# Optimization experiments

Hardware: AMD Instinct MI355X
Metric: run time of the kernel (lower is better)

The kernel has to match this reference:

```python
import jax, jax.numpy as jnp
import numpy as np

ALG = 8  # octonion algebra dimension
_TRIPLES = [(1,2,3),(1,4,5),(1,7,6),(2,4,6),(2,5,7),(3,4,7),(3,6,5)]

def _oct_table():
    # Cayley multiplication table: e_i * e_j = S[i,j] * e_{K[i,j]}
    K = np.zeros((8,8), np.int64); S = np.zeros((8,8), np.int64)
    K[0,:] = np.arange(8); S[0,:] = 1
    K[:,0] = np.arange(8); S[:,0] = 1
    for i in range(1,8):
        K[i,i] = 0; S[i,i] = -1
    for (a,b,c) in _TRIPLES:
        for x,y,z in ((a,b,c),(b,c,a),(c,a,b)):
            K[x,y] = z; S[x,y] = 1
            K[y,x] = z; S[y,x] = -1
    return K, S

_K, _S = _oct_table()

def _ternary(w):
    # BitNet-style absmean ternary quantization (STE is irrelevant for fwd)
    scale = jnp.mean(jnp.abs(w)) + 1e-8
    wq = jnp.clip(jnp.round(w / scale), -1.0, 1.0) * scale
    return w + jax.lax.stop_gradient(wq - w)

def _oct_big(w):
    # w: [8, din8, dout8] -> structured dense [8*din8, 8*dout8]
    # out_k = sum_{i,j: e_i e_j = s e_k} s * x_i @ W_j  (64 static blocks)
    din8, dout8 = w.shape[1], w.shape[2]
    big = jnp.zeros((8, din8, 8, dout8), w.dtype)
    for i in range(8):
        for j in range(8):
            big = big.at[i, :, int(_K[i, j]), :].set(float(_S[i, j]) * w[j])
    return big.reshape(8 * din8, 8 * dout8)

def _oct_linear(x, w):
    return x @ _oct_big(_ternary(w))

def setup_inputs() -> dict:
    key = jax.random.key(0)
    k1, k2, k3, k4 = jax.random.split(key, 4)
    B, T, D = 8, 4096, 768
    H = 2048  # int(2*4*768/3) rounded up to multiple of 8
    d8, h8 = D // ALG, H // ALG
    x = jax.random.normal(k1, (B, T, D), dtype=jnp.float32)
    w_gate = 0.02 * jax.random.normal(k2, (ALG, d8, h8), dtype=jnp.float32)
    w_up   = 0.02 * jax.random.normal(k3, (ALG, d8, h8), dtype=jnp.float32)
    w_down = 0.02 * jax.random.normal(k4, (ALG, h8, d8), dtype=jnp.float32)
    return {"x": x, "w_gate": w_gate, "w_up": w_up, "w_down": w_down}

def reference(x, w_gate, w_up, w_down):
    gate = _oct_linear(x, w_gate)          # [B,T,H]
    up   = _oct_linear(x, w_up)            # [B,T,H]
    h    = jax.nn.silu(gate) * up          # SwiGLU gate
    return _oct_linear(h, w_down)          # [B,T,D]
```

## Files before the change

kernel.cpp:

```cpp
#include <hip/hip_runtime.h>
#include <hip/hip_bf16.h>

typedef unsigned short u16;
typedef unsigned int u32;
typedef float f32x4 __attribute__((ext_vector_type(4)));
typedef __bf16 bf16x8 __attribute__((ext_vector_type(8)));

#define AS1 __attribute__((address_space(1)))
#define AS3 __attribute__((address_space(3)))

#define MTOT 32768
#define DK   768
#define HN   2048

__constant__ signed char J_TAB[64] = {
  0,1,2,3,4,5,6,7,
  1,0,3,2,5,4,7,6,
  2,3,0,1,6,7,4,5,
  3,2,1,0,7,6,5,4,
  4,5,6,7,0,1,2,3,
  5,4,7,6,1,0,3,2,
  6,7,4,5,2,3,0,1,
  7,6,5,4,3,2,1,0};
__constant__ signed char S_TAB[64] = {
   1, 1, 1, 1, 1, 1, 1, 1,
  -1, 1,-1, 1,-1, 1, 1,-1,
  -1, 1, 1,-1,-1,-1, 1, 1,
  -1,-1, 1, 1,-1, 1,-1, 1,
  -1, 1, 1, 1, 1,-1,-1,-1,
  -1,-1, 1,-1, 1, 1, 1,-1,
  -1,-1,-1, 1, 1,-1, 1, 1,
  -1, 1,-1,-1, 1, 1,-1, 1};

__device__ __forceinline__ u16 f2bf(float f) {
  u32 x = __float_as_uint(f);
  x += 0x7fffu + ((x >> 16) & 1u);
  return (u16)(x >> 16);
}

__device__ __forceinline__ void gload_lds16(const void* g, void* l) {
  __builtin_amdgcn_global_load_lds((AS1 void*)(g), (AS3 void*)(l), 16, 0, 0);
}

#define VMW(N) do { __builtin_amdgcn_sched_barrier(0); \
  asm volatile("s_waitcnt vmcnt(" #N ")" ::: "memory"); \
  __builtin_amdgcn_sched_barrier(0); } while (0)
#define BAR() do { __builtin_amdgcn_sched_barrier(0); \
  __builtin_amdgcn_s_barrier(); \
  __builtin_amdgcn_sched_barrier(0); } while (0)

template <int LDK>
__device__ __forceinline__ void stage_half(const u16* __restrict__ src,
                                           u16* lds, int tid) {
#pragma unroll
  for (int f0 = 0; f0 < 1024; f0 += 512) {
    int flat = f0 + tid;
    int row = flat >> 3;
    int c = (flat & 7) ^ (row & 7);
    gload_lds16(src + row * LDK + c * 8, lds + (f0 + (tid & ~63)) * 8);
  }
}

template <int LDK, bool SA, bool SB, int VM>
__device__ __forceinline__ void ktile4(
    const u16* lAp, const u16* lBp, u16* lAn, u16* lBn,
    const u16* __restrict__ aStage, const u16* __restrict__ bStage,
    int tid, int arow, int brow, int c0, int c1, f32x4 (&acc)[8][4]) {
  bf16x8 afr[4][2], bfr[4][2];
#pragma unroll
  for (int mi = 0; mi < 4; ++mi) {
    const u16* p = lAp + (arow + mi * 16) * 64;
    afr[mi][0] = *(const bf16x8*)(p + c0);
    afr[mi][1] = *(const bf16x8*)(p + c1);
  }
#pragma unroll
  for (int ni = 0; ni < 2; ++ni) {
    const u16* p = lBp + (brow + ni * 16) * 64;
    bfr[ni][0] = *(const bf16x8*)(p + c0);
    bfr[ni][1] = *(const bf16x8*)(p + c1);
  }
  if constexpr (SA) stage_half<LDK>(aStage, lAn, tid);
  BAR();
  __builtin_amdgcn_s_setprio(1);
#pragma unroll
  for (int mi = 0; mi < 4; ++mi)
#pragma unroll
    for (int ni = 0; ni < 2; ++ni) {
      acc[mi][ni] = __builtin_amdgcn_mfma_f32_16x16x32_bf16(
          afr[mi][0], bfr[ni][0], acc[mi][ni], 0, 0, 0);
      acc[mi][ni] = __builtin_amdgcn_mfma_f32_16x16x32_bf16(
          afr[mi][1], bfr[ni][1], acc[mi][ni], 0, 0, 0);
    }
  __builtin_amdgcn_s_setprio(0);
  BAR();
#pragma unroll
  for (int ni = 2; ni < 4; ++ni) {
    const u16* p = lBp + (brow + ni * 16) * 64;
    bfr[ni][0] = *(const bf16x8*)(p + c0);
    bfr[ni][1] = *(const bf16x8*)(p + c1);
  }
  if constexpr (SA) stage_half<LDK>(aStage + 128 * LDK, lAn + 128 * 64, tid);
  BAR();
  __builtin_amdgcn_s_setprio(1);
#pragma unroll
  for (int mi = 0; mi < 4; ++mi)
#pragma unroll
    for (int ni = 2; ni < 4; ++ni) {
      acc[mi][ni] = __builtin_amdgcn_mfma_f32_16x16x32_bf16(
          afr[mi][0], bfr[ni][0], acc[mi][ni], 0, 0, 0);
      acc[mi][ni] = __builtin_amdgcn_mfma_f32_16x16x32_bf16(
          afr[mi][1], bfr[ni][1], acc[mi][ni], 0, 0, 0);
    }
  __builtin_amdgcn_s_setprio(0);
  BAR();
#pragma unroll
  for (int mi = 0; mi < 4; ++mi) {
    const u16* p = lAp + (arow + 64 + mi * 16) * 64;
    afr[mi][0] = *(const bf16x8*)(p + c0);
    afr[mi][1] = *(const bf16x8*)(p + c1);
  }
  if constexpr (SB) stage_half<LDK>(bStage, lBn, tid);
  BAR();
  __builtin_amdgcn_s_setprio(1);
#pragma unroll
  for (int mi = 0; mi < 4; ++mi)
#pragma unroll
    for (int ni = 2; ni < 4; ++ni) {
      acc[4 + mi][ni] = __builtin_amdgcn_mfma_f32_16x16x32_bf16(
          afr[mi][0], bfr[ni][0], acc[4 + mi][ni], 0, 0, 0);
      acc[4 + mi][ni] = __builtin_amdgcn_mfma_f32_16x16x32_bf16(
          afr[mi][1], bfr[ni][1], acc[4 + mi][ni], 0, 0, 0);
    }
  __builtin_amdgcn_s_setprio(0);
  BAR();
  if constexpr (SB) stage_half<LDK>(bStage + 128 * LDK, lBn + 128 * 64, tid);
  if constexpr (VM == 4) VMW(4);
  else if constexpr (VM == 0) VMW(0);
  BAR();
  __builtin_amdgcn_s_setprio(1);
#pragma unroll
  for (int mi = 0; mi < 4; ++mi)
#pragma unroll
    for (int ni = 0; ni < 2; ++ni) {
      acc[4 + mi][ni] = __builtin_amdgcn_mfma_f32_16x16x32_bf16(
          afr[mi][0], bfr[ni][0], acc[4 + mi][ni], 0, 0, 0);
      acc[4 + mi][ni] = __builtin_amdgcn_mfma_f32_16x16x32_bf16(
          afr[mi][1], bfr[ni][1], acc[4 + mi][ni], 0, 0, 0);
    }
  __builtin_amdgcn_s_setprio(0);
  BAR();
}

template <int NK, int LDK>
__device__ __forceinline__ void gemm_core(const u16* __restrict__ aSrc,
                                          const u16* __restrict__ bSrc, int tid,
                                          u16* lA0, u16* lA1, u16* lB0, u16* lB1,
                                          f32x4 (&acc)[8][4]) {
  const int lane = tid & 63;
  const int wave = tid >> 6;
  const int wm = wave >> 2, wn = wave & 3;
  const int l15 = lane & 15, quad = (lane >> 4) & 3;
  const int arow = wm * 128 + l15;
  const int brow = wn * 64 + l15;
  const int c0 = (quad ^ (l15 & 7)) * 8;
  const int c1 = ((quad + 4) ^ (l15 & 7)) * 8;

  stage_half<LDK>(aSrc, lA0, tid);
  stage_half<LDK>(aSrc + 128 * LDK, lA0 + 128 * 64, tid);
  stage_half<LDK>(bSrc, lB0, tid);
  stage_half<LDK>(bSrc + 128 * LDK, lB0 + 128 * 64, tid);
  stage_half<LDK>(bSrc + 64, lB1, tid);
  stage_half<LDK>(bSrc + 64 + 128 * LDK, lB1 + 128 * 64, tid);
  VMW(4);
  BAR();

#pragma unroll 1
  for (int i = 0; i < NK / 2 - 1; ++i) {
    ktile4<LDK, true, true, 4>(lA0, lB0, lA1, lB0,
                               aSrc + (2 * i + 1) * 64, bSrc + (2 * i + 2) * 64,
                               tid, arow, brow, c0, c1, acc);
    ktile4<LDK, true, true, 4>(lA1, lB1, lA0, lB1,
                               aSrc + (2 * i + 2) * 64, bSrc + (2 * i + 3) * 64,
                               tid, arow, brow, c0, c1, acc);
  }
  ktile4<LDK, true, false, 0>(lA0, lB0, lA1, lB0,
                              aSrc + (NK - 1) * 64, nullptr,
                              tid, arow, brow, c0, c1, acc);
  ktile4<LDK, false, false, -1>(lA1, lB1, lA0, lB1, nullptr, nullptr,
                                tid, arow, brow, c0, c1, acc);
}

__global__ void scales1_kernel(const float* __restrict__ w0,
                               const float* __restrict__ w1,
                               const float* __restrict__ w2,
                               float* __restrict__ partials) {
  __shared__ float red[256];
  const int t = blockIdx.x / 192;
  const int chunk = blockIdx.x % 192;
  const float* w = (t == 0) ? w0 : (t == 1) ? w1 : w2;
  const float4* w4 = (const float4*)(w + chunk * 1024);
  float4 v = w4[threadIdx.x];
  red[threadIdx.x] = fabsf(v.x) + fabsf(v.y) + fabsf(v.z) + fabsf(v.w);
  __syncthreads();
  for (int off = 128; off; off >>= 1) {
    if (threadIdx.x < off) red[threadIdx.x] += red[threadIdx.x + off];
    __syncthreads();
  }
  if (threadIdx.x == 0) partials[blockIdx.x] = red[0];
}

__global__ void scales2_kernel(const float* __restrict__ partials,
                               float* __restrict__ scales) {
  __shared__ float red[256];
  float s = (threadIdx.x < 192) ? partials[blockIdx.x * 192 + threadIdx.x] : 0.f;
  red[threadIdx.x] = s;
  __syncthreads();
  for (int off = 128; off; off >>= 1) {
    if (threadIdx.x < off) red[threadIdx.x] += red[threadIdx.x + off];
    __syncthreads();
  }
  if (threadIdx.x == 0) scales[blockIdx.x] = red[0] / 196608.f + 1e-8f;
}

__global__ void build_big_kernel(const float* __restrict__ w,
                                 const float* __restrict__ scales, int sidx,
                                 int A, int B, int ilv, u16* __restrict__ dst) {
  int idx = blockIdx.x * 256 + threadIdx.x;
  int K8 = 8 * A;
  int n = idx / K8;
  int k = idx - n * K8;
  int i = k / A, a = k - i * A;
  int c = n / B, b = n - c * B;
  float scale = scales[sidx];
  int j = J_TAB[i * 8 + c];
  float q = rintf(w[(j * A + a) * B + b] / scale);
  q = fminf(1.f, fmaxf(-1.f, q));
  int nd = (ilv < 0) ? n : (((n & ~15) << 1) | (ilv << 4) | (n & 15));
  dst[nd * K8 + k] = f2bf(q * (float)S_TAB[i * 8 + c]);
}

__global__ void cvt_x_kernel(const float* __restrict__ x, u16* __restrict__ xb) {
  int gid = blockIdx.x * 256 + threadIdx.x;
  const float4* x4 = (const float4*)x;
  float4 v0 = x4[gid * 2], v1 = x4[gid * 2 + 1];
  uint4 o;
  o.x = (u32)f2bf(v0.x) | ((u32)f2bf(v0.y) << 16);
  o.y = (u32)f2bf(v0.z) | ((u32)f2bf(v0.w) << 16);
  o.z = (u32)f2bf(v1.x) | ((u32)f2bf(v1.y) << 16);
  o.w = (u32)f2bf(v1.z) | ((u32)f2bf(v1.w) << 16);
  ((uint4*)xb)[gid] = o;
}

__global__ __launch_bounds__(512, 2) void gemm1_kernel(
    const u16* __restrict__ xb, const u16* __restrict__ wgu,
    const float* __restrict__ scales, u16* __restrict__ h) {
  __shared__ __align__(16) u16 lA0[256 * 64], lA1[256 * 64];
  __shared__ __align__(16) u16 lB0[256 * 64], lB1[256 * 64];
  const int tid = threadIdx.x;
  const int logical = (blockIdx.x & 7) * 256 + (blockIdx.x >> 3);
  const int bn = logical & 15;
  const int bm = logical >> 4;
  const int m0 = bm * 256, n0 = bn * 256;

  f32x4 acc[8][4] = {};
  gemm_core<12, DK>(xb + (size_t)m0 * DK, wgu + (size_t)n0 * DK, tid,
                    lA0, lA1, lB0, lB1, acc);

  const int lane = tid & 63, wave = tid >> 6;
  const int wm = wave >> 2, wn = wave & 3;
  const int l15 = lane & 15, quad = lane >> 4;
  const float sg = scales[0], su = scales[1];
  const int hb = bn * 8 + wn * 2;
#pragma unroll
  for (int mi = 0; mi < 8; ++mi)
#pragma unroll
    for (int pr = 0; pr < 2; ++pr) {
      const int hc = (hb + pr) * 16 + l15;
#pragma unroll
      for (int r = 0; r < 4; ++r) {
        int m = m0 + wm * 128 + mi * 16 + quad * 4 + r;
        float g = acc[mi][2 * pr][r] * sg;
        float u = acc[mi][2 * pr + 1][r] * su;
        float hv = g / (1.f + __expf(-g)) * u;
        h[(size_t)m * HN + hc] = f2bf(hv);
      }
    }
}

__global__ __launch_bounds__(512, 2) void gemm2_kernel(
    const u16* __restrict__ h, const u16* __restrict__ wd,
    const float* __restrict__ scales, float* __restrict__ out) {
  __shared__ __align__(16) u16 lA0[256 * 64], lA1[256 * 64];
  __shared__ __align__(16) u16 lB0[256 * 64], lB1[256 * 64];
  const int tid = threadIdx.x;
  const int logical = (blockIdx.x & 7) * 48 + (blockIdx.x >> 3);
  const int bn = logical % 3;
  const int bm = logical / 3;
  const int m0 = bm * 256, n0 = bn * 256;

  f32x4 acc[8][4] = {};
  gemm_core<32, HN>(h + (size_t)m0 * HN, wd + (size_t)n0 * HN, tid,
                    lA0, lA1, lB0, lB1, acc);

  const int lane = tid & 63, wave = tid >> 6;
  const int wm = wave >> 2, wn = wave & 3;
  const int l15 = lane & 15, quad = lane >> 4;
  const float sd = scales[2];
#pragma unroll
  for (int mi = 0; mi < 8; ++mi)
#pragma unroll
    for (int ni = 0; ni < 4; ++ni) {
      const int n = n0 + wn * 64 + ni * 16 + l15;
#pragma unroll
      for (int r = 0; r < 4; ++r) {
        int m = m0 + wm * 128 + mi * 16 + quad * 4 + r;
        out[(size_t)m * DK + n] = acc[mi][ni][r] * sd;
      }
    }
}

extern "C" void kernel_launch(void* const* d_in, const int* in_sizes, int n_in,
                              void* d_out, int out_size, void* d_ws, size_t ws_size,
                              hipStream_t stream) {
  const float* x      = (const float*)d_in[0];
  const float* w_gate = (const float*)d_in[1];
  const float* w_up   = (const float*)d_in[2];
  const float* w_down = (const float*)d_in[3];
  float* out = (float*)d_out;

  char* ws = (char*)d_ws;
  float* scales   = (float*)ws;
  float* partials = (float*)(ws + 256);
  u16* wgu = (u16*)(ws + 4096);
  u16* wd  = (u16*)(ws + 4096 + 6291456u);
  u16* xb  = (u16*)(ws + 4096 + 9437184u);
  u16* h   = (u16*)(ws + 4096 + 9437184u + 50331648u);

  scales1_kernel<<<576, 256, 0, stream>>>(w_gate, w_up, w_down, partials);
  scales2_kernel<<<3, 256, 0, stream>>>(partials, scales);
  build_big_kernel<<<6144, 256, 0, stream>>>(w_gate, scales, 0, 96, 256, 0, wgu);
  build_big_kernel<<<6144, 256, 0, stream>>>(w_up,   scales, 1, 96, 256, 1, wgu);
  build_big_kernel<<<6144, 256, 0, stream>>>(w_down, scales, 2, 256, 96, -1, wd);
  cvt_x_kernel<<<12288, 256, 0, stream>>>(x, xb);
  gemm1_kernel<<<2048, 512, 0, stream>>>(xb, wgu, scales, h);
  gemm2_kernel<<<384, 512, 0, stream>>>(h, wd, scales, out);
}
```

Baseline: 577.2 us.

## Retile down-projection GEMM to 128-row tiles with triple-buffered LDS pipeline

The down-projection GEMM moves from 256x256 tiles with double buffering to 128x256 tiles with a three-stage LDS ring, doubling the grid to 768 blocks to fill the device better. The inner ktile4 is reorganized to load full B fragments up front and issue one MFMA per K-half per phase. gemm1's epilogue writes pairs of bf16 as packed 32-bit stores, with a matching K permutation applied when building the down weight. Together these aim to lift occupancy and store efficiency, at the cost of more register pressure and less reuse per tile.

```diff
diff --git a/kernel.cpp b/kernel.cpp
--- a/kernel.cpp
+++ b/kernel.cpp
@@ -66,71 +66,56 @@
     const u16* lAp, const u16* lBp, u16* lAn, u16* lBn,
     const u16* __restrict__ aStage, const u16* __restrict__ bStage,
     int tid, int arow, int brow, int c0, int c1, f32x4 (&acc)[8][4]) {
-  bf16x8 afr[4][2], bfr[4][2];
-#pragma unroll
-  for (int mi = 0; mi < 4; ++mi) {
-    const u16* p = lAp + (arow + mi * 16) * 64;
-    afr[mi][0] = *(const bf16x8*)(p + c0);
-    afr[mi][1] = *(const bf16x8*)(p + c1);
-  }
-#pragma unroll
-  for (int ni = 0; ni < 2; ++ni) {
-    const u16* p = lBp + (brow + ni * 16) * 64;
-    bfr[ni][0] = *(const bf16x8*)(p + c0);
-    bfr[ni][1] = *(const bf16x8*)(p + c1);
-  }
+  bf16x8 a0[4], a1[4], a2[4], a3[4], b0[4], b1[4];
+#pragma unroll
+  for (int mi = 0; mi < 4; ++mi)
+    a0[mi] = *(const bf16x8*)(lAp + (arow + mi * 16) * 64 + c0);
+#pragma unroll
+  for (int ni = 0; ni < 4; ++ni)
+    b0[ni] = *(const bf16x8*)(lBp + (brow + ni * 16) * 64 + c0);
+#pragma unroll
+  for (int mi = 0; mi < 4; ++mi)
+    a1[mi] = *(const bf16x8*)(lAp + (arow + mi * 16) * 64 + c1);
+#pragma unroll
+  for (int ni = 0; ni < 4; ++ni)
+    b1[ni] = *(const bf16x8*)(lBp + (brow + ni * 16) * 64 + c1);
   if constexpr (SA) stage_half<LDK>(aStage, lAn, tid);
   BAR();
   __builtin_amdgcn_s_setprio(1);
 #pragma unroll
   for (int mi = 0; mi < 4; ++mi)
 #pragma unroll
-    for (int ni = 0; ni < 2; ++ni) {
+    for (int ni = 0; ni < 4; ++ni)
       acc[mi][ni] = __builtin_amdgcn_mfma_f32_16x16x32_bf16(
-          afr[mi][0], bfr[ni][0], acc[mi][ni], 0, 0, 0);
+          a0[mi], b0[ni], acc[mi][ni], 0, 0, 0);
+  __builtin_amdgcn_s_setprio(0);
+  BAR();
+#pragma unroll
+  for (int mi = 0; mi < 4; ++mi)
+    a2[mi] = *(const bf16x8*)(lAp + (arow + 64 + mi * 16) * 64 + c0);
+  if constexpr (SA) stage_half<LDK>(aStage + 128 * LDK, lAn + 128 * 64, tid);
+  BAR();
+  __builtin_amdgcn_s_setprio(1);
+#pragma unroll
+  for (int mi = 0; mi < 4; ++mi)
+#pragma unroll
+    for (int ni = 0; ni < 4; ++ni)
       acc[mi][ni] = __builtin_amdgcn_mfma_f32_16x16x32_bf16(
-          afr[mi][1], bfr[ni][1], acc[mi][ni], 0, 0, 0);
-    }
-  __builtin_amdgcn_s_setprio(0);
-  BAR();
-#pragma unroll
-  for (int ni = 2; ni < 4; ++ni) {
-    const u16* p = lBp + (brow + ni * 16) * 64;
-    bfr[ni][0] = *(const bf16x8*)(p + c0);
-    bfr[ni][1] = *(const bf16x8*)(p + c1);
-  }
-  if constexpr (SA) stage_half<LDK>(aStage + 128 * LDK, lAn + 128 * 64, tid);
-  BAR();
-  __builtin_amdgcn_s_setprio(1);
-#pragma unroll
-  for (int mi = 0; mi < 4; ++mi)
-#pragma unroll
-    for (int ni = 2; ni < 4; ++ni) {
-      acc[mi][ni] = __builtin_amdgcn_mfma_f32_16x16x32_bf16(
-          afr[mi][0], bfr[ni][0], acc[mi][ni], 0, 0, 0);
-      acc[mi][ni] = __builtin_amdgcn_mfma_f32_16x16x32_bf16(
-          afr[mi][1], bfr[ni][1], acc[mi][ni], 0, 0, 0);
-    }
-  __builtin_amdgcn_s_setprio(0);
-  BAR();
-#pragma unroll
-  for (int mi = 0; mi < 4; ++mi) {
-    const u16* p = lAp + (arow + 64 + mi * 16) * 64;
-    afr[mi][0] = *(const bf16x8*)(p + c0);
-    afr[mi][1] = *(const bf16x8*)(p + c1);
-  }
+          a1[mi], b1[ni], acc[mi][ni], 0, 0, 0);
+  __builtin_amdgcn_s_setprio(0);
+  BAR();
+#pragma unroll
+  for (int mi = 0; mi < 4; ++mi)
+    a3[mi] = *(const bf16x8*)(lAp + (arow + 64 + mi * 16) * 64 + c1);
   if constexpr (SB) stage_half<LDK>(bStage, lBn, tid);
   BAR();
   __builtin_amdgcn_s_setprio(1);
 #pragma unroll
   for (int mi = 0; mi < 4; ++mi)
 #pragma unroll
-    for (int ni = 2; ni < 4; ++ni) {
+    for (int ni = 0; ni < 4; ++ni)
       acc[4 + mi][ni] = __builtin_amdgcn_mfma_f32_16x16x32_bf16(
-          afr[mi][0], bfr[ni][0], acc[4 + mi][ni], 0, 0, 0);
-      acc[4 + mi][ni] = __builtin_amdgcn_mfma_f32_16x16x32_bf16(
-          afr[mi][1], bfr[ni][1], acc[4 + mi][ni], 0, 0, 0);
-    }
+          a2[mi], b0[ni], acc[4 + mi][ni], 0, 0, 0);
   __builtin_amdgcn_s_setprio(0);
   BAR();
   if constexpr (SB) stage_half<LDK>(bStage + 128 * LDK, lBn + 128 * 64, tid);
@@ -141,12 +126,9 @@
 #pragma unroll
   for (int mi = 0; mi < 4; ++mi)
 #pragma unroll
-    for (int ni = 0; ni < 2; ++ni) {
+    for (int ni = 0; ni < 4; ++ni)
       acc[4 + mi][ni] = __builtin_amdgcn_mfma_f32_16x16x32_bf16(
-          afr[mi][0], bfr[ni][0], acc[4 + mi][ni], 0, 0, 0);
-      acc[4 + mi][ni] = __builtin_amdgcn_mfma_f32_16x16x32_bf16(
-          afr[mi][1], bfr[ni][1], acc[4 + mi][ni], 0, 0, 0);
-    }
+          a3[mi], b1[ni], acc[4 + mi][ni], 0, 0, 0);
   __builtin_amdgcn_s_setprio(0);
   BAR();
 }
@@ -188,6 +170,53 @@
                               tid, arow, brow, c0, c1, acc);
   ktile4<LDK, false, false, -1>(lA1, lB1, lA0, lB1, nullptr, nullptr,
                                 tid, arow, brow, c0, c1, acc);
+}
+
+template <bool ST, int VM>
+__device__ __forceinline__ void ktile2(
+    const u16* lAp, const u16* lBp, u16* lAs, u16* lBs,
+    const u16* __restrict__ aS, const u16* __restrict__ bS,
+    int tid, int arow, int brow, int c0, int c1, f32x4 (&acc)[4][4]) {
+  bf16x8 a0[4], a1[4], b0[4], b1[4];
+#pragma unroll
+  for (int mi = 0; mi < 4; ++mi)
+    a0[mi] = *(const bf16x8*)(lAp + (arow + mi * 16) * 64 + c0);
+#pragma unroll
+  for (int ni = 0; ni < 4; ++ni)
+    b0[ni] = *(const bf16x8*)(lBp + (brow + ni * 16) * 64 + c0);
+#pragma unroll
+  for (int mi = 0; mi < 4; ++mi)
+    a1[mi] = *(const bf16x8*)(lAp + (arow + mi * 16) * 64 + c1);
+#pragma unroll
+  for (int ni = 0; ni < 4; ++ni)
+    b1[ni] = *(const bf16x8*)(lBp + (brow + ni * 16) * 64 + c1);
+  if constexpr (ST) stage_half<HN>(aS, lAs, tid);
+  BAR();
+  __builtin_amdgcn_s_setprio(1);
+#pragma unroll
+  for (int mi = 0; mi < 4; ++mi)
+#pragma unroll
+    for (int ni = 0; ni < 4; ++ni)
+      acc[mi][ni] = __builtin_amdgcn_mfma_f32_16x16x32_bf16(
+          a0[mi], b0[ni], acc[mi][ni], 0, 0, 0);
+  __builtin_amdgcn_s_setprio(0);
+  BAR();
+  if constexpr (ST) {
+    stage_half<HN>(bS, lBs, tid);
+    stage_half<HN>(bS + 128 * HN, lBs + 128 * 64, tid);
+  }
+  if constexpr (VM == 6) VMW(6);
+  else if constexpr (VM == 0) VMW(0);
+  BAR();
+  __builtin_amdgcn_s_setprio(1);
+#pragma unroll
+  for (int mi = 0; mi < 4; ++mi)
+#pragma unroll
+    for (int ni = 0; ni < 4; ++ni)
+      acc[mi][ni] = __builtin_amdgcn_mfma_f32_16x16x32_bf16(
+          a1[mi], b1[ni], acc[mi][ni], 0, 0, 0);
+  __builtin_amdgcn_s_setprio(0);
+  BAR();
 }
 
 __global__ void scales1_kernel(const float* __restrict__ w0,
@@ -235,8 +264,9 @@
   int j = J_TAB[i * 8 + c];
   float q = rintf(w[(j * A + a) * B + b] / scale);
   q = fminf(1.f, fmaxf(-1.f, q));
-  int nd = (ilv < 0) ? n : (((n & ~15) << 1) | (ilv << 4) | (n & 15));
-  dst[nd * K8 + k] = f2bf(q * (float)S_TAB[i * 8 + c]);
+  int nd = (ilv >= 0) ? (((n & ~15) << 1) | (ilv << 4) | (n & 15)) : n;
+  int kd = (ilv == -2) ? ((k & ~31) | ((k & 15) << 1) | ((k >> 4) & 1)) : k;
+  dst[nd * K8 + kd] = f2bf(q * (float)S_TAB[i * 8 + c]);
 }
 
 __global__ void cvt_x_kernel(const float* __restrict__ x, u16* __restrict__ xb) {
@@ -270,50 +300,78 @@
   const int wm = wave >> 2, wn = wave & 3;
   const int l15 = lane & 15, quad = lane >> 4;
   const float sg = scales[0], su = scales[1];
-  const int hb = bn * 8 + wn * 2;
+  const int a_ = bn * 4 + wn;
+  u32* h32 = (u32*)h;
 #pragma unroll
   for (int mi = 0; mi < 8; ++mi)
 #pragma unroll
-    for (int pr = 0; pr < 2; ++pr) {
-      const int hc = (hb + pr) * 16 + l15;
-#pragma unroll
-      for (int r = 0; r < 4; ++r) {
-        int m = m0 + wm * 128 + mi * 16 + quad * 4 + r;
-        float g = acc[mi][2 * pr][r] * sg;
-        float u = acc[mi][2 * pr + 1][r] * su;
-        float hv = g / (1.f + __expf(-g)) * u;
-        h[(size_t)m * HN + hc] = f2bf(hv);
-      }
+    for (int r = 0; r < 4; ++r) {
+      int m = m0 + wm * 128 + mi * 16 + quad * 4 + r;
+      float g0 = acc[mi][0][r] * sg, u0 = acc[mi][1][r] * su;
+      float g1 = acc[mi][2][r] * sg, u1 = acc[mi][3][r] * su;
+      float h0 = g0 / (1.f + __expf(-g0)) * u0;
+      float h1 = g1 / (1.f + __expf(-g1)) * u1;
+      h32[(size_t)m * (HN / 2) + a_ * 16 + l15] =
+          (u32)f2bf(h0) | ((u32)f2bf(h1) << 16);
     }
 }
 
 __global__ __launch_bounds__(512, 2) void gemm2_kernel(
     const u16* __restrict__ h, const u16* __restrict__ wd,
     const float* __restrict__ scales, float* __restrict__ out) {
-  __shared__ __align__(16) u16 lA0[256 * 64], lA1[256 * 64];
-  __shared__ __align__(16) u16 lB0[256 * 64], lB1[256 * 64];
+  __shared__ __align__(16) u16 lA[3][128 * 64];
+  __shared__ __align__(16) u16 lB[3][256 * 64];
   const int tid = threadIdx.x;
-  const int logical = (blockIdx.x & 7) * 48 + (blockIdx.x >> 3);
+  const int logical = (blockIdx.x & 7) * 96 + (blockIdx.x >> 3);
   const int bn = logical % 3;
   const int bm = logical / 3;
-  const int m0 = bm * 256, n0 = bn * 256;
-
-  f32x4 acc[8][4] = {};
-  gemm_core<32, HN>(h + (size_t)m0 * HN, wd + (size_t)n0 * HN, tid,
-                    lA0, lA1, lB0, lB1, acc);
+  const int m0 = bm * 128, n0 = bn * 256;
+  const u16* aSrc = h + (size_t)m0 * HN;
+  const u16* bSrc = wd + (size_t)n0 * HN;
 
   const int lane = tid & 63, wave = tid >> 6;
   const int wm = wave >> 2, wn = wave & 3;
-  const int l15 = lane & 15, quad = lane >> 4;
+  const int l15 = lane & 15, quad = (lane >> 4) & 3;
+  const int arow = wm * 64 + l15;
+  const int brow = wn * 64 + l15;
+  const int c0 = (quad ^ (l15 & 7)) * 8;
+  const int c1 = ((quad + 4) ^ (l15 & 7)) * 8;
+
+  f32x4 acc[4][4] = {};
+
+  stage_half<HN>(aSrc, lA[0], tid);
+  stage_half<HN>(bSrc, lB[0], tid);
+  stage_half<HN>(bSrc + 128 * HN, lB[0] + 128 * 64, tid);
+  stage_half<HN>(aSrc + 64, lA[1], tid);
+  stage_half<HN>(bSrc + 64, lB[1], tid);
+  stage_half<HN>(bSrc + 64 + 128 * HN, lB[1] + 128 * 64, tid);
+  VMW(6);
+  BAR();
+
+  u16 *pA0 = lA[0], *pA1 = lA[1], *pA2 = lA[2];
+  u16 *pB0 = lB[0], *pB1 = lB[1], *pB2 = lB[2];
+#pragma unroll 1
+  for (int S = 0; S < (HN / 64) - 2; ++S) {
+    ktile2<true, 6>(pA0, pB0, pA2, pB2,
+                    aSrc + (S + 2) * 64, bSrc + (S + 2) * 64,
+                    tid, arow, brow, c0, c1, acc);
+    u16* tA = pA0; pA0 = pA1; pA1 = pA2; pA2 = tA;
+    u16* tB = pB0; pB0 = pB1; pB1 = pB2; pB2 = tB;
+  }
+  ktile2<false, 0>(pA0, pB0, nullptr, nullptr, nullptr, nullptr,
+                   tid, arow, brow, c0, c1, acc);
+  ktile2<false, -1>(pA1, pB1, nullptr, nullptr, nullptr, nullptr,
+                    tid, arow, brow, c0, c1, acc);
+
   const float sd = scales[2];
 #pragma unroll
-  for (int mi = 0; mi < 8; ++mi)
+  for (int mi = 0; mi < 4; ++mi)
 #pragma unroll
     for (int ni = 0; ni < 4; ++ni) {
       const int n = n0 + wn * 64 + ni * 16 + l15;
 #pragma unroll
       for (int r = 0; r < 4; ++r) {
-        int m = m0 + wm * 128 + mi * 16 + quad * 4 + r;
+        int m = m0 + wm * 64 + mi * 16 + quad * 4 + r;
         out[(size_t)m * DK + n] = acc[mi][ni][r] * sd;
       }
     }
@@ -340,8 +398,8 @@
   scales2_kernel<<<3, 256, 0, stream>>>(partials, scales);
   build_big_kernel<<<6144, 256, 0, stream>>>(w_gate, scales, 0, 96, 256, 0, wgu);
   build_big_kernel<<<6144, 256, 0, stream>>>(w_up,   scales, 1, 96, 256, 1, wgu);
-  build_big_kernel<<<6144, 256, 0, stream>>>(w_down, scales, 2, 256, 96, -1, wd);
+  build_big_kernel<<<6144, 256, 0, stream>>>(w_down, scales, 2, 256, 96, -2, wd);
   cvt_x_kernel<<<12288, 256, 0, stream>>>(x, xb);
   gemm1_kernel<<<2048, 512, 0, stream>>>(xb, wgu, scales, h);
-  gemm2_kernel<<<384, 512, 0, stream>>>(h, wd, scales, out);
-}
+  gemm2_kernel<<<768, 512, 0, stream>>>(h, wd, scales, out);
+}
```

Result: faster. 552.1 us (-4.3%).
